# Kernel optimization log

Hardware: AMD Instinct MI355X
Metric: run time of the kernel (lower is better)

## Reference

```python
import jax, jax.numpy as jnp
import numpy as np

B, S, IN_DIM = 8, 4096, 1024
N_SLOTS, SLOT_DIM, N_HEADS, CHUNK, TOP_K = 64, 256, 4, 16, 3
EPS_LN = 1e-5


def setup_inputs() -> dict:
    key = jax.random.key(0)
    ks = jax.random.split(key, 8)
    std = 0.02
    return {
        "x": jax.random.normal(ks[0], (B, S, IN_DIM), jnp.float32),
        "slot_memory": jax.random.normal(ks[1], (1, N_SLOTS, SLOT_DIM), jnp.float32) * std,
        "slot_keys": jax.random.normal(ks[2], (N_SLOTS, SLOT_DIM), jnp.float32) * std,
        "W_in": jax.random.normal(ks[3], (IN_DIM, SLOT_DIM), jnp.float32) / np.sqrt(IN_DIM).astype(np.float32),
        "W_write": jax.random.normal(ks[4], (SLOT_DIM, SLOT_DIM), jnp.float32) / np.sqrt(SLOT_DIM).astype(np.float32),
        "W_gate": jax.random.normal(ks[5], (2 * SLOT_DIM, 1), jnp.float32) / np.sqrt(2 * SLOT_DIM).astype(np.float32),
        "b_gate": jnp.zeros((1,), jnp.float32),
        "W_out": jax.random.normal(ks[6], (SLOT_DIM, IN_DIM), jnp.float32) / np.sqrt(SLOT_DIM).astype(np.float32),
        "ln_in_scale": jnp.ones((IN_DIM,), jnp.float32),
        "ln_in_bias": jnp.zeros((IN_DIM,), jnp.float32),
        "ln_s_scale": jnp.ones((SLOT_DIM,), jnp.float32),
        "ln_s_bias": jnp.zeros((SLOT_DIM,), jnp.float32),
    }


def _layer_norm(x, scale, bias):
    m = jnp.mean(x, axis=-1, keepdims=True)
    v = jnp.mean((x - m) ** 2, axis=-1, keepdims=True)
    return (x - m) * jax.lax.rsqrt(v + EPS_LN) * scale + bias


def _l2norm(x):
    n = jnp.sqrt(jnp.sum(x * x, axis=-1, keepdims=True))
    return x / jnp.maximum(n, 1e-12)  # matches F.normalize eps


def _forward(x, slot_memory, slot_keys, W_in, W_write, W_gate, b_gate, W_out,
             ln_in_scale, ln_in_bias, ln_s_scale, ln_s_bias):
    Bx, Sx, _ = x.shape
    hd = SLOT_DIM // N_HEADS
    slots0 = jnp.broadcast_to(slot_memory, (Bx, N_SLOTS, SLOT_DIM))

    # ---- batched read attention over slots ----
    q = _layer_norm(x, ln_in_scale, ln_in_bias) @ W_in          # (B,S,D)
    qh = q.reshape(Bx, Sx, N_HEADS, hd)
    kh = slots0.reshape(Bx, N_SLOTS, N_HEADS, hd)               # k == v == slots
    scores = jnp.einsum('bshd,bnhd->bhsn', qh, kh) * (hd ** -0.5)
    attn = jax.nn.softmax(scores, axis=-1)                      # (B,H,S,N)
    read = jnp.einsum('bhsn,bnhd->bshd', attn, kh).reshape(Bx, Sx, SLOT_DIM)

    # ---- sequential chunked top-k gather/scatter slot write ----
    key_norms = _l2norm(slot_keys)                              # (N,D)
    b_idx = jnp.arange(Bx)[:, None]

    def chunk_step(slots, chunk):                               # chunk: (B,C,D)
        summary = chunk.mean(axis=1)                            # (B,D)
        match = _l2norm(summary) @ key_norms.T                  # (B,N) cosine sim
        _, top_idx = jax.lax.top_k(match, TOP_K)                # (B,K)
        wv = summary @ W_write                                  # (B,D)
        sel = jnp.take_along_axis(slots, top_idx[:, :, None], axis=1)  # (B,K,D)
        gate = jax.nn.sigmoid(
            jnp.concatenate([sel.mean(axis=1), wv], axis=-1) @ W_gate + b_gate)  # (B,1)
        g = gate[:, None, :]
        new_vals = (1.0 - g) * sel + g * wv[:, None, :]         # (B,K,D)
        return slots.at[b_idx, top_idx].set(new_vals), None

    chunks = read.reshape(Bx, Sx // CHUNK, CHUNK, SLOT_DIM).transpose(1, 0, 2, 3)
    slots_f, _ = jax.lax.scan(chunk_step, slots0, chunks)
    new_slots = _layer_norm(slots_f, ln_s_scale, ln_s_bias)

    out = read @ W_out                                          # dropout is identity in eval
    return out, new_slots


def reference(x, slot_memory, slot_keys, W_in, W_write, W_gate, b_gate, W_out,
              ln_in_scale, ln_in_bias, ln_s_scale, ln_s_bias):
    return _forward(x, slot_memory, slot_keys, W_in, W_write, W_gate, b_gate, W_out,
                    ln_in_scale, ln_in_bias, ln_s_scale, ln_s_bias)
```

## Files before the change

kernel.cpp:

```cpp
#include <hip/hip_runtime.h>

typedef __attribute__((ext_vector_type(8))) short s8v;
typedef __attribute__((ext_vector_type(4))) float f4v;

#define PAD1 88

__device__ __forceinline__ unsigned short f2bf(float f) {
  unsigned u = __float_as_uint(f);
  u += 0x7fffu + ((u >> 16) & 1u);
  return (unsigned short)(u >> 16);
}
__device__ __forceinline__ float bf2f(unsigned short h) {
  return __uint_as_float(((unsigned)h) << 16);
}
__device__ __forceinline__ float rdlanef(float v, int l) {
  return __uint_as_float(__builtin_amdgcn_readlane(__float_as_uint(v), l));
}
__device__ __forceinline__ f4v vmax4(f4v a, f4v b) {
  f4v r; r[0]=fmaxf(a[0],b[0]); r[1]=fmaxf(a[1],b[1]); r[2]=fmaxf(a[2],b[2]); r[3]=fmaxf(a[3],b[3]); return r;
}
__device__ __forceinline__ f4v shflxor4(f4v v, int m) {
  f4v r; r[0]=__shfl_xor(v[0],m); r[1]=__shfl_xor(v[1],m); r[2]=__shfl_xor(v[2],m); r[3]=__shfl_xor(v[3],m); return r;
}
__device__ __forceinline__ f4v exp4(f4v v) {
  f4v r; r[0]=__expf(v[0]); r[1]=__expf(v[1]); r[2]=__expf(v[2]); r[3]=__expf(v[3]); return r;
}

__global__ void k_prep(const float* __restrict__ W_in, const float* __restrict__ lnis,
                       const float* __restrict__ lnib, const float* __restrict__ W_out,
                       const float* __restrict__ skeys, const float* __restrict__ smem0,
                       const float* __restrict__ wgate,
                       unsigned short* __restrict__ wth, unsigned short* __restrict__ wtl,
                       unsigned short* __restrict__ wot, float* __restrict__ keyn,
                       float* __restrict__ d0, float* __restrict__ uvec, float* __restrict__ vvec)
{
  __shared__ float pr[4];
  const int bid = blockIdx.x, tid = threadIdx.x;
  if (bid < 1024) {
    int idx = bid * 256 + tid;
    int n = idx >> 10, k = idx & 1023;
    float val = lnis[k] * W_in[k * 256 + n];
    unsigned short h = f2bf(val);
    wth[idx] = h;
    wtl[idx] = f2bf(val - bf2f(h));
  } else if (bid < 2048) {
    int idx = (bid - 1024) * 256 + tid;
    int n = idx >> 8, k = idx & 255;
    wot[idx] = f2bf(W_out[k * 1024 + n]);
  } else if (bid == 2048) {
    float su = 0.f, sv = 0.f;
    for (int i = 0; i < 1024; ++i) {
      float wv_ = W_in[i * 256 + tid];
      su += lnis[i] * wv_;
      sv += lnib[i] * wv_;
    }
    uvec[tid] = su; vvec[tid] = sv;
  } else {
    int n = bid - 2049;
    float sk = skeys[n * 256 + tid];
    float sq = sk * sk;
    #pragma unroll
    for (int m = 32; m; m >>= 1) sq += __shfl_xor(sq, m);
    if ((tid & 63) == 0) pr[tid >> 6] = sq;
    __syncthreads();
    float tot = pr[0] + pr[1] + pr[2] + pr[3];
    keyn[n * 256 + tid] = sk * (1.0f / fmaxf(sqrtf(tot), 1e-12f));
    float pd = smem0[n * 256 + tid] * wgate[tid];
    #pragma unroll
    for (int m = 32; m; m >>= 1) pd += __shfl_xor(pd, m);
    __syncthreads();
    if ((tid & 63) == 0) pr[tid >> 6] = pd;
    __syncthreads();
    if (tid == 0) d0[n] = pr[0] + pr[1] + pr[2] + pr[3];
  }
}

__global__ void k_stats(const float* __restrict__ x, float* __restrict__ mrow, float* __restrict__ rrow)
{
  const int r = blockIdx.x * 8 + (threadIdx.x >> 5);
  const int j = threadIdx.x & 31;
  const float* p = x + (size_t)r * 1024 + j * 32;
  float s = 0.f, ss = 0.f;
  #pragma unroll
  for (int i = 0; i < 32; i += 4) {
    f4v v = *(const f4v*)(p + i);
    s  += v[0] + v[1] + v[2] + v[3];
    ss += v[0]*v[0] + v[1]*v[1] + v[2]*v[2] + v[3]*v[3];
  }
  #pragma unroll
  for (int m = 16; m; m >>= 1) { s += __shfl_xor(s, m); ss += __shfl_xor(ss, m); }
  if (j == 0) {
    float mean = s * (1.0f / 1024.0f);
    mrow[r] = mean;
    rrow[r] = rsqrtf(ss * (1.0f / 1024.0f) - mean * mean + 1e-5f);
  }
}

__global__ __launch_bounds__(512, 2) void k_gemm1(const float* __restrict__ x,
    const unsigned short* __restrict__ wth, const unsigned short* __restrict__ wtl,
    const float* __restrict__ mrow, const float* __restrict__ rrow,
    const float* __restrict__ uvec, const float* __restrict__ vvec,
    float* __restrict__ q)
{
  __shared__ unsigned short Ah[128 * PAD1], Al[128 * PAD1];
  __shared__ unsigned short Bh[256 * PAD1], Bl[256 * PAD1];
  __shared__ float uls[256], vls[256];
  const int tid = threadIdx.x;
  const int w = tid >> 6, lane = tid & 63;
  const int wm = w >> 2, wn = w & 3;
  const int row0 = blockIdx.x * 128;
  if (tid < 256) { uls[tid] = uvec[tid]; vls[tid] = vvec[tid]; }
  f4v zz = {0.f, 0.f, 0.f, 0.f};
  f4v acc[4][4];
  #pragma unroll
  for (int i = 0; i < 4; ++i)
    #pragma unroll
    for (int j = 0; j < 4; ++j) acc[i][j] = zz;
  const int rowA = tid >> 2, kqA = (tid & 3) * 16;
  const int colB = tid >> 1, khB = (tid & 1) * 32;
  for (int kt = 0; kt < 16; ++kt) {
    const int k0 = kt * 64;
    {
      const float* src = x + (size_t)(row0 + rowA) * 1024 + k0 + kqA;
      float vv[16];
      #pragma unroll
      for (int i = 0; i < 4; ++i) *(f4v*)(vv + 4 * i) = *(const f4v*)(src + 4 * i);
      unsigned short hh[16], ll[16];
      #pragma unroll
      for (int i = 0; i < 16; ++i) {
        unsigned short hsh = f2bf(vv[i]);
        hh[i] = hsh;
        ll[i] = f2bf(vv[i] - bf2f(hsh));
      }
      unsigned short* dh = &Ah[rowA * PAD1 + kqA];
      unsigned short* dl = &Al[rowA * PAD1 + kqA];
      *(s8v*)dh = *(const s8v*)hh; *(s8v*)(dh + 8) = *(const s8v*)(hh + 8);
      *(s8v*)dl = *(const s8v*)ll; *(s8v*)(dl + 8) = *(const s8v*)(ll + 8);
      const unsigned short* sh = wth + (size_t)colB * 1024 + k0 + khB;
      const unsigned short* sl = wtl + (size_t)colB * 1024 + k0 + khB;
      unsigned short* dbh = &Bh[colB * PAD1 + khB];
      unsigned short* dbl = &Bl[colB * PAD1 + khB];
      #pragma unroll
      for (int i = 0; i < 4; ++i) {
        *(s8v*)(dbh + 8 * i) = *(const s8v*)(sh + 8 * i);
        *(s8v*)(dbl + 8 * i) = *(const s8v*)(sl + 8 * i);
      }
    }
    __syncthreads();
    #pragma unroll
    for (int kk = 0; kk < 64; kk += 32) {
      const int kb = kk + (lane >> 4) * 8;
      s8v ah[4], al[4], bh[4], bl[4];
      #pragma unroll
      for (int mi = 0; mi < 4; ++mi) {
        const int rr = (wm * 64 + mi * 16 + (lane & 15)) * PAD1 + kb;
        ah[mi] = *(const s8v*)&Ah[rr];
        al[mi] = *(const s8v*)&Al[rr];
      }
      #pragma unroll
      for (int ni = 0; ni < 4; ++ni) {
        const int ccv = (wn * 64 + ni * 16 + (lane & 15)) * PAD1 + kb;
        bh[ni] = *(const s8v*)&Bh[ccv];
        bl[ni] = *(const s8v*)&Bl[ccv];
      }
      #pragma unroll
      for (int mi = 0; mi < 4; ++mi)
        #pragma unroll
        for (int ni = 0; ni < 4; ++ni) {
          acc[mi][ni] = __builtin_amdgcn_mfma_f32_16x16x32_bf16(ah[mi], bh[ni], acc[mi][ni], 0, 0, 0);
          acc[mi][ni] = __builtin_amdgcn_mfma_f32_16x16x32_bf16(ah[mi], bl[ni], acc[mi][ni], 0, 0, 0);
          acc[mi][ni] = __builtin_amdgcn_mfma_f32_16x16x32_bf16(al[mi], bh[ni], acc[mi][ni], 0, 0, 0);
        }
    }
    __syncthreads();
  }
  #pragma unroll
  for (int mi = 0; mi < 4; ++mi)
    #pragma unroll
    for (int j = 0; j < 4; ++j) {
      const int r = row0 + wm * 64 + mi * 16 + (lane >> 4) * 4 + j;
      const float mv = mrow[r], rv = rrow[r];
      #pragma unroll
      for (int ni = 0; ni < 4; ++ni) {
        const int cidx = wn * 64 + ni * 16 + (lane & 15);
        q[(size_t)r * 256 + cidx] = rv * acc[mi][ni][j] - rv * mv * uls[cidx] + vls[cidx];
      }
    }
}

__global__ __launch_bounds__(512, 2) void k_attn(const float* __restrict__ q,
    const float* __restrict__ smem0, unsigned short* __restrict__ readb,
    float* __restrict__ summ)
{
  __shared__ float Kf[64 * 256];
  __shared__ float Pl[8][16 * 68];
  __shared__ float csm[8][64];
  const int tid = threadIdx.x;
  const int w = tid >> 6, lane = tid & 63;
  const int h = w & 3;
  const int l15 = lane & 15, kq = lane >> 4;

  {
    const int base = tid * 32;
    #pragma unroll
    for (int i = 0; i < 8; ++i)
      *(f4v*)&Kf[base + i * 4] = *(const f4v*)&smem0[base + i * 4];
  }
  __syncthreads();

  s8v bsh[4][2], bsl[4][2], bpv[4][2];
  #pragma unroll
  for (int nt = 0; nt < 4; ++nt)
    #pragma unroll
    for (int ks = 0; ks < 2; ++ks) {
      const float* src = &Kf[(nt * 16 + l15) * 256 + h * 64 + ks * 32 + kq * 8];
      float tmp[8];
      *(f4v*)tmp = *(const f4v*)src; *(f4v*)(tmp + 4) = *(const f4v*)(src + 4);
      unsigned short hh[8], ll[8];
      #pragma unroll
      for (int j = 0; j < 8; ++j) {
        hh[j] = f2bf(tmp[j]);
        ll[j] = f2bf(tmp[j] - bf2f(hh[j]));
      }
      bsh[nt][ks] = *(const s8v*)hh;
      bsl[nt][ks] = *(const s8v*)ll;
      unsigned short pp[8];
      #pragma unroll
      for (int j = 0; j < 8; ++j)
        pp[j] = f2bf(Kf[(ks * 32 + kq * 8 + j) * 256 + h * 64 + nt * 16 + l15]);
      bpv[nt][ks] = *(const s8v*)pp;
    }

  const int g0 = blockIdx.x * 8 + (w >> 2) * 4;
  f4v qv[2][4];
  {
    #pragma unroll
    for (int ks = 0; ks < 2; ++ks) {
      const float* qp = q + (size_t)(g0 * 16 + l15) * 256 + h * 64 + ks * 32 + kq * 8;
      qv[0][ks * 2] = *(const f4v*)qp;
      qv[0][ks * 2 + 1] = *(const f4v*)(qp + 4);
    }
  }
  #pragma unroll
  for (int i = 0; i < 4; ++i) {
    const int cur = i & 1, nxt = cur ^ 1;
    if (i < 3) {
      const int gn = g0 + i + 1;
      #pragma unroll
      for (int ks = 0; ks < 2; ++ks) {
        const float* qp = q + (size_t)(gn * 16 + l15) * 256 + h * 64 + ks * 32 + kq * 8;
        qv[nxt][ks * 2] = *(const f4v*)qp;
        qv[nxt][ks * 2 + 1] = *(const f4v*)(qp + 4);
      }
    }
    const int g = g0 + i;
    s8v ah[2], al[2];
    #pragma unroll
    for (int ks = 0; ks < 2; ++ks) {
      float tmp[8];
      *(f4v*)tmp = qv[cur][ks * 2]; *(f4v*)(tmp + 4) = qv[cur][ks * 2 + 1];
      unsigned short hh[8], ll[8];
      #pragma unroll
      for (int j = 0; j < 8; ++j) {
        hh[j] = f2bf(tmp[j]);
        ll[j] = f2bf(tmp[j] - bf2f(hh[j]));
      }
      ah[ks] = *(const s8v*)hh; al[ks] = *(const s8v*)ll;
    }
    f4v zz = {0.f, 0.f, 0.f, 0.f};
    f4v sacc[4] = {zz, zz, zz, zz};
    #pragma unroll
    for (int ks = 0; ks < 2; ++ks)
      #pragma unroll
      for (int nt = 0; nt < 4; ++nt) {
        sacc[nt] = __builtin_amdgcn_mfma_f32_16x16x32_bf16(ah[ks], bsh[nt][ks], sacc[nt], 0, 0, 0);
        sacc[nt] = __builtin_amdgcn_mfma_f32_16x16x32_bf16(ah[ks], bsl[nt][ks], sacc[nt], 0, 0, 0);
        sacc[nt] = __builtin_amdgcn_mfma_f32_16x16x32_bf16(al[ks], bsh[nt][ks], sacc[nt], 0, 0, 0);
      }
    #pragma unroll
    for (int nt = 0; nt < 4; ++nt) sacc[nt] = sacc[nt] * 0.125f;
    f4v mx = vmax4(vmax4(sacc[0], sacc[1]), vmax4(sacc[2], sacc[3]));
    #pragma unroll
    for (int m = 1; m <= 8; m <<= 1) mx = vmax4(mx, shflxor4(mx, m));
    f4v p[4];
    f4v psum = zz;
    #pragma unroll
    for (int nt = 0; nt < 4; ++nt) { p[nt] = exp4(sacc[nt] - mx); psum = psum + p[nt]; }
    #pragma unroll
    for (int m = 1; m <= 8; m <<= 1) psum = psum + shflxor4(psum, m);
    f4v rs;
    rs[0] = 1.0f / psum[0]; rs[1] = 1.0f / psum[1];
    rs[2] = 1.0f / psum[2]; rs[3] = 1.0f / psum[3];
    #pragma unroll
    for (int nt = 0; nt < 4; ++nt) p[nt] = p[nt] * rs;
    float cs4[4];
    #pragma unroll
    for (int nt = 0; nt < 4; ++nt) {
      cs4[nt] = p[nt][0] + p[nt][1] + p[nt][2] + p[nt][3];
      cs4[nt] += __shfl_xor(cs4[nt], 16);
      cs4[nt] += __shfl_xor(cs4[nt], 32);
    }
    if (kq == 0) {
      #pragma unroll
      for (int nt = 0; nt < 4; ++nt) csm[w][nt * 16 + l15] = cs4[nt];
    }
    #pragma unroll
    for (int nt = 0; nt < 4; ++nt)
      #pragma unroll
      for (int j = 0; j < 4; ++j)
        Pl[w][(kq * 4 + j) * 68 + nt * 16 + l15] = p[nt][j];
    s8v pa[2];
    #pragma unroll
    for (int ks = 0; ks < 2; ++ks) {
      const float* pp = &Pl[w][l15 * 68 + ks * 32 + kq * 8];
      float tmp[8];
      *(f4v*)tmp = *(const f4v*)pp; *(f4v*)(tmp + 4) = *(const f4v*)(pp + 4);
      unsigned short uu[8];
      #pragma unroll
      for (int j = 0; j < 8; ++j) uu[j] = f2bf(tmp[j]);
      pa[ks] = *(const s8v*)uu;
    }
    f4v racc[4] = {zz, zz, zz, zz};
    #pragma unroll
    for (int ks = 0; ks < 2; ++ks)
      #pragma unroll
      for (int nt = 0; nt < 4; ++nt)
        racc[nt] = __builtin_amdgcn_mfma_f32_16x16x32_bf16(pa[ks], bpv[nt][ks], racc[nt], 0, 0, 0);
    const int rowbase = (g >> 8) * 4096 + (g & 255) * 16;
    #pragma unroll
    for (int nt = 0; nt < 4; ++nt)
      #pragma unroll
      for (int j = 0; j < 4; ++j)
        readb[(size_t)(rowbase + kq * 4 + j) * 256 + h * 64 + nt * 16 + l15] = f2bf(racc[nt][j]);
    float s = 0.f;
    #pragma unroll 8
    for (int n = 0; n < 64; ++n) s += csm[w][n] * Kf[n * 256 + h * 64 + lane];
    summ[(size_t)g * 256 + h * 64 + lane] = s * (1.0f / 16.0f);
  }
}

__global__ void k_match(const float* __restrict__ summ, const float* __restrict__ keyn,
                        const float* __restrict__ Wwr, const float* __restrict__ wgate,
                        int* __restrict__ top3, float* __restrict__ wv,
                        float* __restrict__ wg2, float* __restrict__ dwv)
{
  __shared__ float sm[4][256];
  __shared__ float nrm_inv[4];
  __shared__ float mtch[4][64];
  __shared__ float redA[4][4], redB[4][4];
  const int tid = threadIdx.x, lane = tid & 63, w = tid >> 6;
  const int gbase = blockIdx.x * 4;
  #pragma unroll
  for (int gi = 0; gi < 4; ++gi) sm[gi][tid] = summ[(size_t)(gbase + gi) * 256 + tid];
  __syncthreads();
  {
    float ss = 0.f;
    #pragma unroll
    for (int i = 0; i < 4; ++i) { float vv_ = sm[w][lane + i * 64]; ss += vv_ * vv_; }
    #pragma unroll
    for (int m = 32; m; m >>= 1) ss += __shfl_xor(ss, m);
    if (lane == 0) nrm_inv[w] = 1.0f / fmaxf(sqrtf(ss), 1e-12f);
  }
  __syncthreads();
  {
    const int n = tid >> 2, qq = tid & 3;
    float mac[4] = {0.f, 0.f, 0.f, 0.f};
    const float* kp = keyn + n * 256 + qq * 64;
    for (int d = 0; d < 64; ++d) {
      float kv = kp[d];
      int dd = qq * 64 + d;
      mac[0] += sm[0][dd] * kv; mac[1] += sm[1][dd] * kv;
      mac[2] += sm[2][dd] * kv; mac[3] += sm[3][dd] * kv;
    }
    #pragma unroll
    for (int gi = 0; gi < 4; ++gi) {
      float v2_ = mac[gi];
      v2_ += __shfl_xor(v2_, 1);
      v2_ += __shfl_xor(v2_, 2);
      if (qq == 0) mtch[gi][n] = v2_ * nrm_inv[gi];
    }
  }
  __syncthreads();
  {
    float vorig = mtch[w][lane];
    #pragma unroll
    for (int it = 0; it < 3; ++it) {
      float rv = vorig; int ri = lane;
      #pragma unroll
      for (int m = 32; m; m >>= 1) {
        float ov = __shfl_xor(rv, m); int oi = __shfl_xor(ri, m);
        if (ov > rv || (ov == rv && oi < ri)) { rv = ov; ri = oi; }
      }
      if (lane == 0) top3[(gbase + w) * 4 + it] = ri;
      if (lane == ri) vorig = -3.0e38f;
    }
  }
  float wva[4] = {0.f, 0.f, 0.f, 0.f};
  for (int d = 0; d < 256; ++d) {
    float ww = Wwr[(size_t)d * 256 + tid];
    wva[0] += sm[0][d] * ww; wva[1] += sm[1][d] * ww;
    wva[2] += sm[2][d] * ww; wva[3] += sm[3][d] * ww;
  }
  const float g1 = wgate[tid], g2 = wgate[256 + tid];
  #pragma unroll
  for (int gi = 0; gi < 4; ++gi) {
    wv[(size_t)(gbase + gi) * 256 + tid] = wva[gi];
    float p2 = wva[gi] * g2, p1 = wva[gi] * g1;
    #pragma unroll
    for (int m = 32; m; m >>= 1) { p2 += __shfl_xor(p2, m); p1 += __shfl_xor(p1, m); }
    if (lane == 0) { redA[gi][w] = p2; redB[gi][w] = p1; }
  }
  __syncthreads();
  if (tid < 4) {
    wg2[gbase + tid] = redA[tid][0] + redA[tid][1] + redA[tid][2] + redA[tid][3];
    dwv[gbase + tid] = redB[tid][0] + redB[tid][1] + redB[tid][2] + redB[tid][3];
  }
}

__global__ __launch_bounds__(1024) void k_scan(const float* __restrict__ d0,
    const int* __restrict__ top3, const float* __restrict__ wg2, const float* __restrict__ dwv,
    const float* __restrict__ bgate, const float* __restrict__ wv,
    const float* __restrict__ smem0, const float* __restrict__ lnss,
    const float* __restrict__ lnsb, float* __restrict__ outns)
{
  __shared__ float gls[256];
  __shared__ float Wl[256][64];
  __shared__ float pn[64];
  __shared__ float wvs[32][256];
  const int bb = blockIdx.x, tid = threadIdx.x;

  if (tid < 64) {
    const int lane = tid;
    const float bg = bgate[0];
    float dn = d0[lane];
    unsigned long long mk[4];
    #pragma unroll
    for (int j = 0; j < 4; ++j) {
      const int c0 = j * 64;
      const int4 t3 = *(const int4*)&top3[(bb * 256 + c0 + lane) * 4];
      const int ixj = t3.x, iyj = t3.y, izj = t3.z;
      const float wzj = wg2[bb * 256 + c0 + lane] + bg;
      const float dvj = dwv[bb * 256 + c0 + lane];
      unsigned long long mkj = 0ull;
      float gout = 0.f;
      #pragma unroll 1
      for (int sl = 0; sl < 64; ++sl) {
        const int i0 = __builtin_amdgcn_readlane(ixj, sl);
        const int i1 = __builtin_amdgcn_readlane(iyj, sl);
        const int i2 = __builtin_amdgcn_readlane(izj, sl);
        const float wz = rdlanef(wzj, sl);
        const float dv = rdlanef(dvj, sl);
        const float s3 = rdlanef(dn, i0) + rdlanef(dn, i1) + rdlanef(dn, i2);
        const float z = s3 * (1.0f / 3.0f) + wz;
        const float gv = 1.0f / (1.0f + __expf(-z));
        if (lane == sl) gout = gv;
        const bool hit = (lane == i0) | (lane == i1) | (lane == i2);
        mkj |= ((unsigned long long)hit) << sl;
        dn = hit ? (1.0f - gv) * dn + gv * dv : dn;
      }
      gls[c0 + lane] = gout;
      mk[j] = mkj;
    }
    float running = 1.0f;
    #pragma unroll
    for (int j = 3; j >= 0; --j) {
      const unsigned long long mkj = mk[j];
      #pragma unroll 1
      for (int sl = 63; sl >= 0; --sl) {
        const int c = j * 64 + sl;
        const bool hit = (mkj >> sl) & 1ull;
        const float gv = gls[c];
        Wl[c][lane] = hit ? gv * running : 0.f;
        running = hit ? running * (1.0f - gv) : running;
      }
    }
    pn[lane] = running;
  }
  __syncthreads();

  const int n = tid >> 4, dq = tid & 15;
  float acc[16];
  {
    const float p = pn[n];
    const float* v0p = smem0 + n * 256 + dq * 16;
    #pragma unroll
    for (int i = 0; i < 16; i += 4) {
      f4v v0 = *(const f4v*)(v0p + i);
      acc[i] = p * v0[0]; acc[i + 1] = p * v0[1];
      acc[i + 2] = p * v0[2]; acc[i + 3] = p * v0[3];
    }
  }
  const int rr = tid >> 5, cc8 = (tid & 31) * 8;
  for (int ct = 0; ct < 8; ++ct) {
    __syncthreads();
    {
      const float* src = wv + (size_t)(bb * 256 + ct * 32 + rr) * 256 + cc8;
      *(f4v*)&wvs[rr][cc8] = *(const f4v*)src;
      *(f4v*)&wvs[rr][cc8 + 4] = *(const f4v*)(src + 4);
    }
    __syncthreads();
    #pragma unroll 1
    for (int cc = 0; cc < 32; ++cc) {
      const float coef = Wl[ct * 32 + cc][n];
      if (coef != 0.f) {
        const float* wp = &wvs[cc][dq * 16];
        #pragma unroll
        for (int i4 = 0; i4 < 4; ++i4) {
          f4v wq = *(const f4v*)(wp + i4 * 4);
          acc[i4 * 4 + 0] += coef * wq[0];
          acc[i4 * 4 + 1] += coef * wq[1];
          acc[i4 * 4 + 2] += coef * wq[2];
          acc[i4 * 4 + 3] += coef * wq[3];
        }
      }
    }
  }

  float s1 = 0.f;
  #pragma unroll
  for (int i = 0; i < 16; ++i) s1 += acc[i];
  #pragma unroll
  for (int m = 1; m < 16; m <<= 1) s1 += __shfl_xor(s1, m);
  const float mean = s1 * (1.0f / 256.0f);
  float s2 = 0.f;
  #pragma unroll
  for (int i = 0; i < 16; ++i) { float dd = acc[i] - mean; s2 += dd * dd; }
  #pragma unroll
  for (int m = 1; m < 16; m <<= 1) s2 += __shfl_xor(s2, m);
  const float rstd = rsqrtf(s2 * (1.0f / 256.0f) + 1e-5f);
  {
    const int base = (bb * 64 + n) * 256 + dq * 16;
    #pragma unroll
    for (int i = 0; i < 16; ++i) {
      int dd = dq * 16 + i;
      outns[base + i] = (acc[i] - mean) * rstd * lnss[dd] + lnsb[dd];
    }
  }
}

__global__ __launch_bounds__(512, 2) void k_gemm2(const unsigned short* __restrict__ a,
    const unsigned short* __restrict__ wot, float* __restrict__ out)
{
  __shared__ unsigned short As[128 * PAD1];
  __shared__ unsigned short Bs[256 * PAD1];
  const int tid = threadIdx.x;
  const int w = tid >> 6, lane = tid & 63;
  const int wm = w >> 2, wn = w & 3;
  const int mblk = blockIdx.x >> 2, nblk = blockIdx.x & 3;
  const int row0 = mblk * 128, n0 = nblk * 256;
  f4v zz = {0.f, 0.f, 0.f, 0.f};
  f4v acc[4][4];
  #pragma unroll
  for (int i = 0; i < 4; ++i)
    #pragma unroll
    for (int j = 0; j < 4; ++j) acc[i][j] = zz;
  const int rowA = tid >> 2, kqA = (tid & 3) * 16;
  const int colB = tid >> 1, khB = (tid & 1) * 32;
  for (int kt = 0; kt < 4; ++kt) {
    const int k0 = kt * 64;
    {
      const unsigned short* src = a + (size_t)(row0 + rowA) * 256 + k0 + kqA;
      *(s8v*)&As[rowA * PAD1 + kqA] = *(const s8v*)src;
      *(s8v*)&As[rowA * PAD1 + kqA + 8] = *(const s8v*)(src + 8);
      const unsigned short* sb = wot + (size_t)(n0 + colB) * 256 + k0 + khB;
      unsigned short* db = &Bs[colB * PAD1 + khB];
      #pragma unroll
      for (int i = 0; i < 4; ++i) *(s8v*)(db + 8 * i) = *(const s8v*)(sb + 8 * i);
    }
    __syncthreads();
    #pragma unroll
    for (int kk = 0; kk < 64; kk += 32) {
      const int kb = kk + (lane >> 4) * 8;
      s8v af[4], bf[4];
      #pragma unroll
      for (int mi = 0; mi < 4; ++mi)
        af[mi] = *(const s8v*)&As[(wm * 64 + mi * 16 + (lane & 15)) * PAD1 + kb];
      #pragma unroll
      for (int ni = 0; ni < 4; ++ni)
        bf[ni] = *(const s8v*)&Bs[(wn * 64 + ni * 16 + (lane & 15)) * PAD1 + kb];
      #pragma unroll
      for (int mi = 0; mi < 4; ++mi)
        #pragma unroll
        for (int ni = 0; ni < 4; ++ni)
          acc[mi][ni] = __builtin_amdgcn_mfma_f32_16x16x32_bf16(af[mi], bf[ni], acc[mi][ni], 0, 0, 0);
    }
    __syncthreads();
  }
  #pragma unroll
  for (int mi = 0; mi < 4; ++mi)
    #pragma unroll
    for (int j = 0; j < 4; ++j) {
      const int r = row0 + wm * 64 + mi * 16 + (lane >> 4) * 4 + j;
      #pragma unroll
      for (int ni = 0; ni < 4; ++ni) {
        const int cidx = wn * 64 + ni * 16 + (lane & 15);
        out[(size_t)r * 1024 + n0 + cidx] = acc[mi][ni][j];
      }
    }
}

extern "C" void kernel_launch(void* const* d_in, const int* in_sizes, int n_in,
                              void* d_out, int out_size, void* d_ws, size_t ws_size,
                              hipStream_t stream) {
  const float* x      = (const float*)d_in[0];
  const float* smem   = (const float*)d_in[1];
  const float* skeys  = (const float*)d_in[2];
  const float* W_in   = (const float*)d_in[3];
  const float* W_wr   = (const float*)d_in[4];
  const float* wgate  = (const float*)d_in[5];
  const float* bgate  = (const float*)d_in[6];
  const float* W_out  = (const float*)d_in[7];
  const float* lnis   = (const float*)d_in[8];
  const float* lnib   = (const float*)d_in[9];
  const float* lnss   = (const float*)d_in[10];
  const float* lnsb   = (const float*)d_in[11];
  (void)in_sizes; (void)n_in; (void)out_size; (void)ws_size;

  char* ws = (char*)d_ws;
  float*          q_buf = (float*)(ws + 0);
  unsigned short* readb = (unsigned short*)(ws + 134217728);
  float*          summ  = (float*)(ws + 150994944);
  float*          wv    = (float*)(ws + 153092096);
  unsigned short* wth   = (unsigned short*)(ws + 155189248);
  unsigned short* wtl   = (unsigned short*)(ws + 155713536);
  unsigned short* wot   = (unsigned short*)(ws + 156237824);
  float*          keyn  = (float*)(ws + 156762112);
  float*          mrow  = (float*)(ws + 156827648);
  float*          rrow  = (float*)(ws + 156958720);
  float*          uvec  = (float*)(ws + 157089792);
  float*          vvec  = (float*)(ws + 157090816);
  float*          d0    = (float*)(ws + 157091840);
  int*            top3  = (int*)(ws + 157092096);
  float*          wg2   = (float*)(ws + 157124864);
  float*          dwv   = (float*)(ws + 157133056);

  float* out   = (float*)d_out;
  float* outns = out + 33554432;

  k_prep<<<dim3(2113), dim3(256), 0, stream>>>(W_in, lnis, lnib, W_out, skeys, smem, wgate,
                                               wth, wtl, wot, keyn, d0, uvec, vvec);
  k_stats<<<dim3(4096), dim3(256), 0, stream>>>(x, mrow, rrow);
  k_gemm1<<<dim3(256), dim3(512), 0, stream>>>(x, wth, wtl, mrow, rrow, uvec, vvec, q_buf);
  k_attn<<<dim3(256), dim3(512), 0, stream>>>(q_buf, smem, readb, summ);
  k_match<<<dim3(512), dim3(256), 0, stream>>>(summ, keyn, W_wr, wgate, top3, wv, wg2, dwv);
  k_scan<<<dim3(8), dim3(1024), 0, stream>>>(d0, top3, wg2, dwv, bgate, wv, smem, lnss, lnsb, outns);
  k_gemm2<<<dim3(1024), dim3(512), 0, stream>>>(readb, wot, out);
}
```

Before: 364.2 us.

## Fuse LayerNorm row stats into GEMM1 and software-pipeline the slot scan

Row mean and variance for the input LayerNorm are now accumulated inside k_gemm1 while it already loads x, so the separate k_stats kernel and its second 128MB pass over x go away. The serial slot-update scan in k_scan is restructured to prefetch the next step's indices and slot values one iteration ahead, patching them with the previous update. It also uses exp2/rcp intrinsics for the sigmoid and recomputes hit masks in the backward pass instead of storing them. The scan pipelining adds bookkeeping and slightly changes numerics through the fast exp and reciprocal.

```diff
diff --git a/kernel.cpp b/kernel.cpp
--- a/kernel.cpp
+++ b/kernel.cpp
@@ -75,36 +75,15 @@
   }
 }
 
-__global__ void k_stats(const float* __restrict__ x, float* __restrict__ mrow, float* __restrict__ rrow)
-{
-  const int r = blockIdx.x * 8 + (threadIdx.x >> 5);
-  const int j = threadIdx.x & 31;
-  const float* p = x + (size_t)r * 1024 + j * 32;
-  float s = 0.f, ss = 0.f;
-  #pragma unroll
-  for (int i = 0; i < 32; i += 4) {
-    f4v v = *(const f4v*)(p + i);
-    s  += v[0] + v[1] + v[2] + v[3];
-    ss += v[0]*v[0] + v[1]*v[1] + v[2]*v[2] + v[3]*v[3];
-  }
-  #pragma unroll
-  for (int m = 16; m; m >>= 1) { s += __shfl_xor(s, m); ss += __shfl_xor(ss, m); }
-  if (j == 0) {
-    float mean = s * (1.0f / 1024.0f);
-    mrow[r] = mean;
-    rrow[r] = rsqrtf(ss * (1.0f / 1024.0f) - mean * mean + 1e-5f);
-  }
-}
-
 __global__ __launch_bounds__(512, 2) void k_gemm1(const float* __restrict__ x,
     const unsigned short* __restrict__ wth, const unsigned short* __restrict__ wtl,
-    const float* __restrict__ mrow, const float* __restrict__ rrow,
     const float* __restrict__ uvec, const float* __restrict__ vvec,
     float* __restrict__ q)
 {
   __shared__ unsigned short Ah[128 * PAD1], Al[128 * PAD1];
   __shared__ unsigned short Bh[256 * PAD1], Bl[256 * PAD1];
   __shared__ float uls[256], vls[256];
+  __shared__ float mls[128], rls[128];
   const int tid = threadIdx.x;
   const int w = tid >> 6, lane = tid & 63;
   const int wm = w >> 2, wn = w & 3;
@@ -118,6 +97,7 @@
     for (int j = 0; j < 4; ++j) acc[i][j] = zz;
   const int rowA = tid >> 2, kqA = (tid & 3) * 16;
   const int colB = tid >> 1, khB = (tid & 1) * 32;
+  float ps = 0.f, pss = 0.f;
   for (int kt = 0; kt < 16; ++kt) {
     const int k0 = kt * 64;
     {
@@ -128,6 +108,7 @@
       unsigned short hh[16], ll[16];
       #pragma unroll
       for (int i = 0; i < 16; ++i) {
+        ps += vv[i]; pss += vv[i] * vv[i];
         unsigned short hsh = f2bf(vv[i]);
         hh[i] = hsh;
         ll[i] = f2bf(vv[i] - bf2f(hsh));
@@ -174,12 +155,24 @@
     }
     __syncthreads();
   }
+  {
+    float s0 = ps, s1 = pss;
+    s0 += __shfl_xor(s0, 1); s1 += __shfl_xor(s1, 1);
+    s0 += __shfl_xor(s0, 2); s1 += __shfl_xor(s1, 2);
+    if ((tid & 3) == 0) {
+      float mean = s0 * (1.0f / 1024.0f);
+      mls[rowA] = mean;
+      rls[rowA] = rsqrtf(s1 * (1.0f / 1024.0f) - mean * mean + 1e-5f);
+    }
+  }
+  __syncthreads();
   #pragma unroll
   for (int mi = 0; mi < 4; ++mi)
     #pragma unroll
     for (int j = 0; j < 4; ++j) {
-      const int r = row0 + wm * 64 + mi * 16 + (lane >> 4) * 4 + j;
-      const float mv = mrow[r], rv = rrow[r];
+      const int lr = wm * 64 + mi * 16 + (lane >> 4) * 4 + j;
+      const int r = row0 + lr;
+      const float mv = mls[lr], rv = rls[lr];
       #pragma unroll
       for (int ni = 0; ni < 4; ++ni) {
         const int cidx = wn * 64 + ni * 16 + (lane & 15);
@@ -423,7 +416,6 @@
     const float* __restrict__ smem0, const float* __restrict__ lnss,
     const float* __restrict__ lnsb, float* __restrict__ outns)
 {
-  __shared__ float gls[256];
   __shared__ float Wl[256][64];
   __shared__ float pn[64];
   __shared__ float wvs[32][256];
@@ -432,45 +424,75 @@
   if (tid < 64) {
     const int lane = tid;
     const float bg = bgate[0];
+    const float L2E = 1.4426950408889634f;
+    const float COEFN = -0.48089834696298783f;
+    int ixA[4], iyA[4], izA[4];
+    float wzA[4], dvA[4], goA[4];
+    #pragma unroll
+    for (int j = 0; j < 4; ++j) {
+      const int c = j * 64 + lane;
+      int4 t3 = *(const int4*)&top3[(bb * 256 + c) * 4];
+      ixA[j] = t3.x; iyA[j] = t3.y; izA[j] = t3.z;
+      wzA[j] = -(wg2[bb * 256 + c] + bg) * L2E;
+      dvA[j] = dwv[bb * 256 + c];
+      goA[j] = 0.f;
+    }
     float dn = d0[lane];
-    unsigned long long mk[4];
+    int i0p = 255, i1p = 255, i2p = 255;
+    float gp = 0.f, dvp = 0.f;
+    int i0c = __builtin_amdgcn_readlane(ixA[0], 0);
+    int i1c = __builtin_amdgcn_readlane(iyA[0], 0);
+    int i2c = __builtin_amdgcn_readlane(izA[0], 0);
+    float wzc = rdlanef(wzA[0], 0), dvc = rdlanef(dvA[0], 0);
+    float P0 = rdlanef(dn, i0c), P1 = rdlanef(dn, i1c), P2 = rdlanef(dn, i2c);
+
+    auto step = [&](int sl, int nix, int niy, int niz, float nwz, float ndv,
+                    int nsl, bool dopull, float& goref) {
+      float m0 = (i0c == i0p || i0c == i1p || i0c == i2p) ? gp : 0.f;
+      float m1 = (i1c == i0p || i1c == i1p || i1c == i2p) ? gp : 0.f;
+      float m2 = (i2c == i0p || i2c == i1p || i2c == i2p) ? gp : 0.f;
+      P0 = fmaf(m0, dvp - P0, P0);
+      P1 = fmaf(m1, dvp - P1, P1);
+      P2 = fmaf(m2, dvp - P2, P2);
+      float s3 = P0 + P1 + P2;
+      float e = __builtin_amdgcn_exp2f(fmaf(s3, COEFN, wzc));
+      float g = __builtin_amdgcn_rcpf(1.0f + e);
+      goref = (lane == sl) ? g : goref;
+      bool hit = (lane == i0p) | (lane == i1p) | (lane == i2p);
+      float ml = hit ? gp : 0.f;
+      dn = fmaf(ml, dvp - dn, dn);
+      i0p = i0c; i1p = i1c; i2p = i2c; gp = g; dvp = dvc;
+      if (dopull) {
+        i0c = __builtin_amdgcn_readlane(nix, nsl);
+        i1c = __builtin_amdgcn_readlane(niy, nsl);
+        i2c = __builtin_amdgcn_readlane(niz, nsl);
+        wzc = rdlanef(nwz, nsl); dvc = rdlanef(ndv, nsl);
+        P0 = rdlanef(dn, i0c); P1 = rdlanef(dn, i1c); P2 = rdlanef(dn, i2c);
+      }
+    };
+
     #pragma unroll
     for (int j = 0; j < 4; ++j) {
-      const int c0 = j * 64;
-      const int4 t3 = *(const int4*)&top3[(bb * 256 + c0 + lane) * 4];
-      const int ixj = t3.x, iyj = t3.y, izj = t3.z;
-      const float wzj = wg2[bb * 256 + c0 + lane] + bg;
-      const float dvj = dwv[bb * 256 + c0 + lane];
-      unsigned long long mkj = 0ull;
-      float gout = 0.f;
       #pragma unroll 1
-      for (int sl = 0; sl < 64; ++sl) {
-        const int i0 = __builtin_amdgcn_readlane(ixj, sl);
-        const int i1 = __builtin_amdgcn_readlane(iyj, sl);
-        const int i2 = __builtin_amdgcn_readlane(izj, sl);
-        const float wz = rdlanef(wzj, sl);
-        const float dv = rdlanef(dvj, sl);
-        const float s3 = rdlanef(dn, i0) + rdlanef(dn, i1) + rdlanef(dn, i2);
-        const float z = s3 * (1.0f / 3.0f) + wz;
-        const float gv = 1.0f / (1.0f + __expf(-z));
-        if (lane == sl) gout = gv;
-        const bool hit = (lane == i0) | (lane == i1) | (lane == i2);
-        mkj |= ((unsigned long long)hit) << sl;
-        dn = hit ? (1.0f - gv) * dn + gv * dv : dn;
-      }
-      gls[c0 + lane] = gout;
-      mk[j] = mkj;
-    }
+      for (int sl = 0; sl < 63; ++sl)
+        step(sl, ixA[j], iyA[j], izA[j], wzA[j], dvA[j], sl + 1, true, goA[j]);
+      if (j < 3)
+        step(63, ixA[j + 1], iyA[j + 1], izA[j + 1], wzA[j + 1], dvA[j + 1], 0, true, goA[j]);
+      else
+        step(63, ixA[3], iyA[3], izA[3], wzA[3], dvA[3], 0, false, goA[j]);
+    }
+
     float running = 1.0f;
     #pragma unroll
     for (int j = 3; j >= 0; --j) {
-      const unsigned long long mkj = mk[j];
       #pragma unroll 1
       for (int sl = 63; sl >= 0; --sl) {
-        const int c = j * 64 + sl;
-        const bool hit = (mkj >> sl) & 1ull;
-        const float gv = gls[c];
-        Wl[c][lane] = hit ? gv * running : 0.f;
+        const int a0 = __builtin_amdgcn_readlane(ixA[j], sl);
+        const int a1 = __builtin_amdgcn_readlane(iyA[j], sl);
+        const int a2 = __builtin_amdgcn_readlane(izA[j], sl);
+        const float gv = rdlanef(goA[j], sl);
+        const bool hit = (lane == a0) | (lane == a1) | (lane == a2);
+        Wl[j * 64 + sl][lane] = hit ? gv * running : 0.f;
         running = hit ? running * (1.0f - gv) : running;
       }
     }
@@ -625,8 +647,6 @@
   unsigned short* wtl   = (unsigned short*)(ws + 155713536);
   unsigned short* wot   = (unsigned short*)(ws + 156237824);
   float*          keyn  = (float*)(ws + 156762112);
-  float*          mrow  = (float*)(ws + 156827648);
-  float*          rrow  = (float*)(ws + 156958720);
   float*          uvec  = (float*)(ws + 157089792);
   float*          vvec  = (float*)(ws + 157090816);
   float*          d0    = (float*)(ws + 157091840);
@@ -639,8 +659,7 @@
 
   k_prep<<<dim3(2113), dim3(256), 0, stream>>>(W_in, lnis, lnib, W_out, skeys, smem, wgate,
                                                wth, wtl, wot, keyn, d0, uvec, vvec);
-  k_stats<<<dim3(4096), dim3(256), 0, stream>>>(x, mrow, rrow);
-  k_gemm1<<<dim3(256), dim3(512), 0, stream>>>(x, wth, wtl, mrow, rrow, uvec, vvec, q_buf);
+  k_gemm1<<<dim3(256), dim3(512), 0, stream>>>(x, wth, wtl, uvec, vvec, q_buf);
   k_attn<<<dim3(256), dim3(512), 0, stream>>>(q_buf, smem, readb, summ);
   k_match<<<dim3(512), dim3(256), 0, stream>>>(summ, keyn, W_wr, wgate, top3, wv, wg2, dwv);
   k_scan<<<dim3(8), dim3(1024), 0, stream>>>(d0, top3, wg2, dwv, bgate, wv, smem, lnss, lnsb, outns);
```

Result: no change. 364.4 us (+0.1%).
